# Optimization experiments

Hardware: AMD Instinct MI355X
Metric: run time of the kernel (lower is better)

Reference implementation:

```python
import jax, jax.numpy as jnp
import numpy as np

B, T, D, H, R = 4, 4096, 1024, 16, 256
DH = D // H  # 64


def setup_inputs() -> dict:
    key = jax.random.key(0)
    ks = jax.random.split(key, 5)
    s = 0.02
    return {
        "x": jax.random.normal(ks[0], (B, T, D), dtype=jnp.float32),
        "Wq": jax.random.normal(ks[1], (D, D), dtype=jnp.float32) * s,
        "bq": jnp.zeros((D,), dtype=jnp.float32),
        "Wd": jax.random.normal(ks[2], (D, R), dtype=jnp.float32) * s,
        "bd": jnp.zeros((R,), dtype=jnp.float32),
        "Wu": jax.random.normal(ks[3], (R, 2 * D), dtype=jnp.float32) * s,
        "bu": jnp.zeros((2 * D,), dtype=jnp.float32),
        "Wo": jax.random.normal(ks[4], (D, D), dtype=jnp.float32) * s,
        "bo": jnp.zeros((D,), dtype=jnp.float32),
    }


def reference(x, Wq, bq, Wd, bd, Wu, bu, Wo, bo):
    b, t = x.shape[0], x.shape[1]
    # q projection -> (B,T,H,DH)
    q = (x @ Wq + bq).reshape(b, t, H, DH)
    # low-rank KV: down then up -> (B,T,H,2*DH)
    kv = ((x @ Wd + bd) @ Wu + bu).reshape(b, t, H, 2 * DH)
    k, v = kv[..., :DH], kv[..., DH:]
    # elu+1 feature map
    q = jax.nn.elu(q) + 1.0
    k = jax.nn.elu(k) + 1.0
    # linear attention: context = k^T v per head -> (B,H,DH,DH)
    context = jnp.einsum("bthd,bthe->bhde", k, v)
    out = jnp.einsum("bthd,bhde->bthe", q, context)  # (B,T,H,DH)
    # normalizer: q . sum_t(k)
    k_sum = k.sum(axis=1)  # (B,H,DH)
    z = 1.0 / (jnp.einsum("bthd,bhd->bth", q, k_sum) + 1e-6)
    out = out * z[..., None]
    return out.reshape(b, t, D) @ Wo + bo
```

## Files before the change

kernel.cpp:

```cpp
#include <hip/hip_runtime.h>
#include <hip/hip_bf16.h>
#include <cstddef>
#include <cstdint>

#define B_  4
#define T_  4096
#define D_  1024
#define H_  16
#define DH_ 64
#define R_  256
#define BT_ (B_ * T_)
#define TWO_D_ (2 * D_)

typedef __attribute__((ext_vector_type(8))) short short8;
typedef __attribute__((ext_vector_type(4))) float f32x4;

__device__ __forceinline__ float elu1(float x) {
    return x > 0.0f ? x + 1.0f : __expf(x);
}

__device__ __forceinline__ float bf2f(short u) {
    union { uint32_t i; float f; } c;
    c.i = ((uint32_t)(uint16_t)u) << 16;
    return c.f;
}

typedef __attribute__((address_space(1))) void void_g;
typedef __attribute__((address_space(3))) void void_l;
__device__ __forceinline__ void gld_lds16(const void* g, void* l) {
    __builtin_amdgcn_global_load_lds(
        (const void_g*)(uintptr_t)g,
        (void_l*)(uint32_t)(uintptr_t)l,
        16, 0, 0);
}

__device__ __forceinline__ void store_out(float* p, float v) { *p = v; }
__device__ __forceinline__ void store_out(__hip_bfloat16* p, float v) { *p = __float2bfloat16(v); }

#define PBM 256
#define PBN 256

template<int EPI, bool BROW, typename OT>
__global__ __launch_bounds__(512, 2) void gemm_p8(
    const __hip_bfloat16* __restrict__ A,
    const __hip_bfloat16* __restrict__ Bt,
    const float* __restrict__ bias,
    OT* __restrict__ C,
    int M, int N, int K)
{
    __shared__ alignas(16) __hip_bfloat16 sm[65536];
    __hip_bfloat16* Asm = sm;
    __hip_bfloat16* Bsm = sm + 32768;

    const int nbx = N / PBN;
    const int nbm = M / PBM;
    const int sh = (nbm < 8) ? nbm : 8;
    const int id = blockIdx.x;
    const int wi = id % (sh * nbx);
    const int bm = ((id / (sh * nbx)) * sh + (wi % sh)) * PBM;
    const int bn = (wi / sh) * PBN;

    const int tid  = threadIdx.x;
    const int lane = tid & 63;
    const int w    = tid >> 6;
    const int wm   = w >> 2;
    const int wn   = w & 3;
    const int r15  = lane & 15;
    const int kg   = lane >> 4;

    const int nt = K / 64;

    const int rl = tid >> 3;
    const int g  = (tid & 7) ^ (rl & 7);
    const __hip_bfloat16* aS = A  + (size_t)(bm + rl) * K + g * 8;
    const __hip_bfloat16* bS = Bt + (size_t)(bn + rl) * K + g * 8;
    __hip_bfloat16* dA = Asm + tid * 8;
    __hip_bfloat16* dB = Bsm + tid * 8;

    auto stA = [&](int t, int h) {
        const int tc = (t < nt) ? t : (nt - 1);
        __hip_bfloat16* d = dA + ((t & 1) * 2 + h) * 8192;
        const __hip_bfloat16* s = aS + (size_t)(h * 128) * K + tc * 64;
        gld_lds16(s, d);
        gld_lds16(s + (size_t)64 * K, d + 4096);
    };
    auto stB = [&](int t, int h) {
        const int tc = (t < nt) ? t : (nt - 1);
        __hip_bfloat16* d = dB + ((t & 1) * 2 + h) * 8192;
        const __hip_bfloat16* s = bS + (size_t)(h * 128) * K + tc * 64;
        gld_lds16(s, d);
        gld_lds16(s + (size_t)64 * K, d + 4096);
    };

    const int x3    = (r15 & 7) << 3;
    const int kofs0 = (kg * 8) ^ x3;
    const int kofs1 = (32 + kg * 8) ^ x3;
    const __hip_bfloat16* Af0 = Asm + wm * 8192 + r15 * 64;
    const __hip_bfloat16* Bf0 = Bsm + (wn >> 1) * 8192 + (wn & 1) * 4096 + r15 * 64;
    const __hip_bfloat16* Af1 = Af0 + 16384;
    const __hip_bfloat16* Bf1 = Bf0 + 16384;

    f32x4 acc[8][4] = {};
    short8 af[8][2], bf[4][2];

#define RDA(i, ks, BASE) af[i][ks] = *(const short8*)((BASE) + (i) * 1024 + ((ks) ? kofs1 : kofs0))
#define RDB(j, ks, BASE) bf[j][ks] = *(const short8*)((BASE) + (j) * 1024 + ((ks) ? kofs1 : kofs0))
#define MM(ILO, IHI, JLO, JHI, KS)                                             \
    _Pragma("unroll")                                                          \
    for (int i = (ILO); i < (IHI); ++i)                                        \
        _Pragma("unroll")                                                      \
        for (int j = (JLO); j < (JHI); ++j)                                    \
            acc[i][j] = __builtin_amdgcn_mfma_f32_16x16x32_bf16(af[i][KS], bf[j][KS], acc[i][j], 0, 0, 0)
#define SB0() __builtin_amdgcn_sched_barrier(0)

    stA(0, 0); stA(0, 1); stB(0, 0); stB(0, 1); stA(1, 0); stA(1, 1);
    asm volatile("s_waitcnt vmcnt(4)" ::: "memory");
    __builtin_amdgcn_s_barrier();

    for (int t = 0; t < nt; t += 2) {
#pragma unroll
        for (int i = 0; i < 4; ++i) RDA(i, 0, Af0);
#pragma unroll
        for (int j = 0; j < 2; ++j) RDB(j, 0, Bf0);
        SB0();
#pragma unroll
        for (int i = 0; i < 4; ++i) RDA(i, 1, Af0);
#pragma unroll
        for (int j = 0; j < 2; ++j) RDB(j, 1, Bf0);
        stB(t + 1, 0);
        __builtin_amdgcn_s_barrier();
        asm volatile("s_waitcnt lgkmcnt(6)" ::: "memory");
        SB0();
        __builtin_amdgcn_s_setprio(1);
        MM(0, 4, 0, 2, 0);
        asm volatile("s_waitcnt lgkmcnt(0)" ::: "memory");
        SB0();
        MM(0, 4, 0, 2, 1);
        __builtin_amdgcn_s_setprio(0);
        __builtin_amdgcn_s_barrier();

#pragma unroll
        for (int i = 4; i < 8; ++i) RDA(i, 0, Af0);
        SB0();
#pragma unroll
        for (int i = 4; i < 8; ++i) RDA(i, 1, Af0);
        stB(t + 1, 1);
        __builtin_amdgcn_s_barrier();
        asm volatile("s_waitcnt lgkmcnt(4)" ::: "memory");
        SB0();
        __builtin_amdgcn_s_setprio(1);
        MM(4, 8, 0, 2, 0);
        asm volatile("s_waitcnt lgkmcnt(0)" ::: "memory");
        SB0();
        MM(4, 8, 0, 2, 1);
        __builtin_amdgcn_s_setprio(0);
        __builtin_amdgcn_s_barrier();

#pragma unroll
        for (int j = 2; j < 4; ++j) RDB(j, 0, Bf0);
        SB0();
#pragma unroll
        for (int j = 2; j < 4; ++j) RDB(j, 1, Bf0);
        stA(t + 2, 0);
        __builtin_amdgcn_s_barrier();
        asm volatile("s_waitcnt lgkmcnt(2)" ::: "memory");
        SB0();
        __builtin_amdgcn_s_setprio(1);
        MM(4, 8, 2, 4, 0);
        asm volatile("s_waitcnt lgkmcnt(0)" ::: "memory");
        SB0();
        MM(4, 8, 2, 4, 1);
        __builtin_amdgcn_s_setprio(0);
        __builtin_amdgcn_s_barrier();

        stA(t + 2, 1);
        asm volatile("s_waitcnt vmcnt(4)" ::: "memory");
        __builtin_amdgcn_s_barrier();
        SB0();
        __builtin_amdgcn_s_setprio(1);
        MM(0, 4, 2, 4, 0);
        MM(0, 4, 2, 4, 1);
        __builtin_amdgcn_s_setprio(0);
        __builtin_amdgcn_s_barrier();

#pragma unroll
        for (int i = 0; i < 4; ++i) RDA(i, 0, Af1);
#pragma unroll
        for (int j = 0; j < 2; ++j) RDB(j, 0, Bf1);
        SB0();
#pragma unroll
        for (int i = 0; i < 4; ++i) RDA(i, 1, Af1);
#pragma unroll
        for (int j = 0; j < 2; ++j) RDB(j, 1, Bf1);
        stB(t + 2, 0);
        __builtin_amdgcn_s_barrier();
        asm volatile("s_waitcnt lgkmcnt(6)" ::: "memory");
        SB0();
        __builtin_amdgcn_s_setprio(1);
        MM(0, 4, 0, 2, 0);
        asm volatile("s_waitcnt lgkmcnt(0)" ::: "memory");
        SB0();
        MM(0, 4, 0, 2, 1);
        __builtin_amdgcn_s_setprio(0);
        __builtin_amdgcn_s_barrier();

#pragma unroll
        for (int i = 4; i < 8; ++i) RDA(i, 0, Af1);
        SB0();
#pragma unroll
        for (int i = 4; i < 8; ++i) RDA(i, 1, Af1);
        stB(t + 2, 1);
        __builtin_amdgcn_s_barrier();
        asm volatile("s_waitcnt lgkmcnt(4)" ::: "memory");
        SB0();
        __builtin_amdgcn_s_setprio(1);
        MM(4, 8, 0, 2, 0);
        asm volatile("s_waitcnt lgkmcnt(0)" ::: "memory");
        SB0();
        MM(4, 8, 0, 2, 1);
        __builtin_amdgcn_s_setprio(0);
        __builtin_amdgcn_s_barrier();

#pragma unroll
        for (int j = 2; j < 4; ++j) RDB(j, 0, Bf1);
        SB0();
#pragma unroll
        for (int j = 2; j < 4; ++j) RDB(j, 1, Bf1);
        stA(t + 3, 0);
        __builtin_amdgcn_s_barrier();
        asm volatile("s_waitcnt lgkmcnt(2)" ::: "memory");
        SB0();
        __builtin_amdgcn_s_setprio(1);
        MM(4, 8, 2, 4, 0);
        asm volatile("s_waitcnt lgkmcnt(0)" ::: "memory");
        SB0();
        MM(4, 8, 2, 4, 1);
        __builtin_amdgcn_s_setprio(0);
        __builtin_amdgcn_s_barrier();

        stA(t + 3, 1);
        asm volatile("s_waitcnt vmcnt(4)" ::: "memory");
        __builtin_amdgcn_s_barrier();
        SB0();
        __builtin_amdgcn_s_setprio(1);
        MM(0, 4, 2, 4, 0);
        MM(0, 4, 2, 4, 1);
        __builtin_amdgcn_s_setprio(0);
        __builtin_amdgcn_s_barrier();
    }
    asm volatile("s_waitcnt vmcnt(0)" ::: "memory");

#undef RDA
#undef RDB
#undef MM
#undef SB0

    const int row0 = bm + wm * 128 + (lane >> 4) * 4;

    float brow[8][4];
    if (BROW) {
#pragma unroll
        for (int i = 0; i < 8; ++i)
#pragma unroll
            for (int r = 0; r < 4; ++r) brow[i][r] = bias[row0 + i * 16 + r];
    }
#pragma unroll
    for (int j = 0; j < 4; ++j) {
        const int col = bn + wn * 64 + j * 16 + r15;
        const float bv = BROW ? 0.0f : bias[col];
        const bool kp_col = ((col & 127) < 64);
#pragma unroll
        for (int i = 0; i < 8; ++i) {
#pragma unroll
            for (int r = 0; r < 4; ++r) {
                const int row = row0 + i * 16 + r;
                float v = acc[i][j][r] + (BROW ? brow[i][r] : bv);
                if (EPI == 1) v = elu1(v);
                else if (EPI == 2) {
                    const bool kp = BROW ? ((row & 127) < 64) : kp_col;
                    if (kp) v = elu1(v);
                }
                store_out(C + (size_t)row * N + col, v);
            }
        }
    }
}

#define BM 128
#define BN 128
#define BK 32
#define NBUF 5

template<int EPI, bool BROW, typename OT>
__global__ __launch_bounds__(256) void gemm_bf16(
    const __hip_bfloat16* __restrict__ A,
    const __hip_bfloat16* __restrict__ Bt,
    const float* __restrict__ bias,
    OT* __restrict__ C,
    OT* __restrict__ C2,
    int M, int N, int K)
{
    __shared__ alignas(16) __hip_bfloat16 As[NBUF * BM * BK];
    __shared__ alignas(16) __hip_bfloat16 Bs[NBUF * BN * BK];

    const int nbx = N / BN;
    const int id = blockIdx.x;
    const int strip = id / (8 * nbx);
    const int wi = id % (8 * nbx);
    const int bm = (strip * 8 + (wi & 7)) * BM;
    const int bn = (wi >> 3) * BN;

    const int tid  = threadIdx.x;
    const int lane = tid & 63;
    const int wm   = (tid >> 7) * 64;
    const int wn   = ((tid >> 6) & 1) * 64;
    const int r15  = lane & 15;
    const int kg   = lane >> 4;

    f32x4 acc[4][4] = {};

    const int c0 = tid, c1 = tid + 256;
    const __hip_bfloat16* a0 = A  + (size_t)(bm + (c0 >> 2)) * K + (c0 & 3) * 8;
    const __hip_bfloat16* a1 = A  + (size_t)(bm + (c1 >> 2)) * K + (c1 & 3) * 8;
    const __hip_bfloat16* b0 = Bt + (size_t)(bn + (c0 >> 2)) * K + (c0 & 3) * 8;
    const __hip_bfloat16* b1 = Bt + (size_t)(bn + (c1 >> 2)) * K + (c1 & 3) * 8;

    const int nk = K / BK;

    auto stage = [&](int t) {
        const int buf = t % NBUF;
        __hip_bfloat16* Ad = As + buf * (BM * BK);
        __hip_bfloat16* Bd = Bs + buf * (BN * BK);
        const int k0 = t * BK;
        gld_lds16(a0 + k0, Ad + c0 * 8);
        gld_lds16(a1 + k0, Ad + c1 * 8);
        gld_lds16(b0 + k0, Bd + c0 * 8);
        gld_lds16(b1 + k0, Bd + c1 * 8);
    };

    stage(0); stage(1); stage(2);

    for (int t = 0; t < nk; ++t) {
        if (t + 3 < nk) {
            stage(t + 3);
            asm volatile("s_waitcnt vmcnt(12)\ns_barrier" ::: "memory");
        } else if (t + 2 < nk) {
            asm volatile("s_waitcnt vmcnt(8)\ns_barrier" ::: "memory");
        } else if (t + 1 < nk) {
            asm volatile("s_waitcnt vmcnt(4)\ns_barrier" ::: "memory");
        } else {
            asm volatile("s_waitcnt vmcnt(0)\ns_barrier" ::: "memory");
        }

        const __hip_bfloat16* Asb = As + (t % NBUF) * (BM * BK);
        const __hip_bfloat16* Bsb = Bs + (t % NBUF) * (BN * BK);

        short8 af[4], bf[4];
#pragma unroll
        for (int i = 0; i < 4; ++i) {
            af[i] = *(const short8*)(Asb + (wm + i * 16 + r15) * BK + kg * 8);
            bf[i] = *(const short8*)(Bsb + (wn + i * 16 + r15) * BK + kg * 8);
        }
#pragma unroll
        for (int i = 0; i < 4; ++i)
#pragma unroll
            for (int j = 0; j < 4; ++j)
                acc[i][j] = __builtin_amdgcn_mfma_f32_16x16x32_bf16(af[i], bf[j], acc[i][j], 0, 0, 0);
    }

    const int row0 = bm + wm + (lane >> 4) * 4;

    if (EPI == 3) {
        const bool qreg = (bn < 1024);
#pragma unroll
        for (int j = 0; j < 4; ++j) {
            const int col = bn + wn + j * 16 + r15;
            const float bv = bias[col];
#pragma unroll
            for (int i = 0; i < 4; ++i)
#pragma unroll
                for (int r = 0; r < 4; ++r) {
                    const int row = row0 + i * 16 + r;
                    float v = acc[i][j][r] + bv;
                    if (qreg) {
                        store_out(C + (size_t)row * 1024 + col, elu1(v));
                    } else {
                        store_out(C2 + (size_t)row * 256 + (col - 1024), v);
                    }
                }
        }
        return;
    }

    float brow[4][4];
    if (BROW) {
#pragma unroll
        for (int i = 0; i < 4; ++i)
#pragma unroll
            for (int r = 0; r < 4; ++r) brow[i][r] = bias[row0 + i * 16 + r];
    }
#pragma unroll
    for (int j = 0; j < 4; ++j) {
        const int col = bn + wn + j * 16 + r15;
        const float bv = BROW ? 0.0f : bias[col];
        const bool kp_col = ((col & 127) < 64);
#pragma unroll
        for (int i = 0; i < 4; ++i) {
#pragma unroll
            for (int r = 0; r < 4; ++r) {
                const int row = row0 + i * 16 + r;
                float v = acc[i][j][r] + (BROW ? brow[i][r] : bv);
                if (EPI == 1) v = elu1(v);
                else if (EPI == 2) {
                    const bool kp = BROW ? ((row & 127) < 64) : kp_col;
                    if (kp) v = elu1(v);
                }
                store_out(C + (size_t)row * N + col, v);
            }
        }
    }
}

__device__ __forceinline__ void tcast_body(
    const float* __restrict__ W, __hip_bfloat16* __restrict__ Wt,
    int K, int N, int bx, int by, int tid, float (*t)[33])
{
    const int n0 = bx * 32, k0 = by * 32;
    const int c = tid & 31, r = tid >> 5;
#pragma unroll
    for (int rr = r; rr < 32; rr += 8)
        t[rr][c] = W[(size_t)(k0 + rr) * N + n0 + c];
    __syncthreads();
#pragma unroll
    for (int rr = r; rr < 32; rr += 8)
        Wt[(size_t)(n0 + rr) * K + k0 + c] = __float2bfloat16(t[c][rr]);
}

__global__ __launch_bounds__(256) void prep(
    const float* __restrict__ x,
    const float* __restrict__ Wq, const float* __restrict__ Wd,
    const float* __restrict__ Wu, const float* __restrict__ Wo,
    __hip_bfloat16* __restrict__ xb,
    __hip_bfloat16* __restrict__ WqdT, __hip_bfloat16* __restrict__ WuT,
    __hip_bfloat16* __restrict__ WoT,
    float* __restrict__ zbase)
{
    __shared__ float t[32][33];
    const int id = blockIdx.x;
    const int tid = threadIdx.x;

    if (id < 8192) {
        const int i = (id * 256 + tid) * 8;
        float4 v0 = *(const float4*)(x + i);
        float4 v1 = *(const float4*)(x + i + 4);
        __hip_bfloat16 tt[8];
        tt[0] = __float2bfloat16(v0.x); tt[1] = __float2bfloat16(v0.y);
        tt[2] = __float2bfloat16(v0.z); tt[3] = __float2bfloat16(v0.w);
        tt[4] = __float2bfloat16(v1.x); tt[5] = __float2bfloat16(v1.y);
        tt[6] = __float2bfloat16(v1.z); tt[7] = __float2bfloat16(v1.w);
        *(short8*)(xb + i) = *(const short8*)tt;
    } else if (id < 8192 + 1024) {
        const int u = id - 8192;
        tcast_body(Wq, WqdT, D_, D_, u & 31, u >> 5, tid, t);
    } else if (id < 8192 + 1280) {
        const int u = id - (8192 + 1024);
        tcast_body(Wd, WqdT + (size_t)D_ * D_, D_, R_, u & 7, u >> 3, tid, t);
    } else if (id < 8192 + 1792) {
        const int u = id - (8192 + 1280);
        tcast_body(Wu, WuT, R_, TWO_D_, u & 63, u >> 6, tid, t);
    } else if (id < 8192 + 2816) {
        const int u = id - (8192 + 1792);
        tcast_body(Wo, WoT, D_, D_, u & 31, u >> 5, tid, t);
    } else {
        const int u = id - (8192 + 2816);
        const int i = (u * 256 + tid) * 8;
        float4 z = {0.f, 0.f, 0.f, 0.f};
        *(float4*)(zbase + i) = z;
        *(float4*)(zbase + i + 4) = z;
    }
}

#define CHT 512

__global__ __launch_bounds__(256) void ctx_mfma(
    const __hip_bfloat16* __restrict__ kvT, float* __restrict__ ctx,
    float* __restrict__ ksum)
{
    __shared__ alignas(16) unsigned char smem[40960];
    float* red0 = (float*)smem;
    float* red1 = (float*)(smem + 20480);

    const int bh = blockIdx.x >> 3;
    const int chunk = blockIdx.x & 7;
    const int b = bh >> 4;
    const int h = bh & 15;
    const int tid = threadIdx.x;
    const int lane = tid & 63;
    const int w = tid >> 6;
    const int r15 = lane & 15;
    const int kg  = lane >> 4;

    f32x4 acc[4][4] = {};
    f32x4 acc4[4] = {};

    const short one = (short)0x3F80;
    const short8 bfv = (r15 == 0)
        ? (short8){one, one, one, one, one, one, one, one}
        : (short8){0, 0, 0, 0, 0, 0, 0, 0};

    const size_t tbase = (size_t)b * T_ + (size_t)chunk * CHT;
    const __hip_bfloat16* src = kvT + (size_t)(h * 128) * BT_ + tbase;

    for (int it = 0; it < CHT / 128; ++it) {
#pragma unroll
        for (int r = 0; r < 8; ++r) {
            const int c = r * 256 + tid;
            const int s = c >> 9, j = (c >> 2) & 127, u = c & 3;
            gld_lds16(src + (size_t)j * BT_ + it * 128 + s * 32 + u * 8,
                      smem + c * 16);
        }
        __syncthreads();

        const __hip_bfloat16* Ls = (const __hip_bfloat16*)smem;
        short8 af[4], bf[4];
#pragma unroll
        for (int i = 0; i < 4; ++i) {
            af[i] = *(const short8*)(Ls + (w * 128 + i * 16 + r15) * 32 + kg * 8);
            bf[i] = *(const short8*)(Ls + (w * 128 + 64 + i * 16 + r15) * 32 + kg * 8);
        }
#pragma unroll
        for (int i = 0; i < 4; ++i) {
#pragma unroll
            for (int j = 0; j < 4; ++j)
                acc[i][j] = __builtin_amdgcn_mfma_f32_16x16x32_bf16(af[i], bf[j], acc[i][j], 0, 0, 0);
            acc4[i] = __builtin_amdgcn_mfma_f32_16x16x32_bf16(af[i], bfv, acc4[i], 0, 0, 0);
        }
        __syncthreads();
    }

    const int q4 = lane >> 4;
    auto wr = [&](float* reg) {
#pragma unroll
        for (int i = 0; i < 4; ++i) {
#pragma unroll
            for (int r = 0; r < 4; ++r) {
                const int row = i * 16 + q4 * 4 + r;
#pragma unroll
                for (int j = 0; j < 4; ++j) reg[row * 80 + j * 16 + r15] = acc[i][j][r];
                reg[row * 80 + 64 + r15] = acc4[i][r];
            }
        }
    };
    auto rd = [&](const float* reg) {
#pragma unroll
        for (int i = 0; i < 4; ++i) {
#pragma unroll
            for (int r = 0; r < 4; ++r) {
                const int row = i * 16 + q4 * 4 + r;
#pragma unroll
                for (int j = 0; j < 4; ++j) acc[i][j][r] += reg[row * 80 + j * 16 + r15];
                acc4[i][r] += reg[row * 80 + 64 + r15];
            }
        }
    };

    if (w == 1) wr(red0);
    if (w == 3) wr(red1);
    __syncthreads();
    if (w == 0) rd(red0);
    if (w == 2) rd(red1);
    __syncthreads();
    if (w == 2) wr(red0);
    __syncthreads();
    if (w == 0) { rd(red0); wr(red0); }
    __syncthreads();

    float* cdst = ctx + (size_t)bh * 4096;
#pragma unroll
    for (int r = 0; r < 16; ++r) {
        const int idx = r * 256 + tid;
        const int d = idx >> 6, e = idx & 63;
        atomicAdd(cdst + idx, red0[d * 80 + e]);
    }
    if (tid < 64) atomicAdd(ksum + bh * 64 + tid, red0[tid * 80 + 64]);
}

__global__ __launch_bounds__(256) void pack_ctx(
    const float* __restrict__ ctx, __hip_bfloat16* __restrict__ ctxT)
{
    __shared__ float L[64 * 65];
    const int bh = blockIdx.x;
    const int tid = threadIdx.x;
#pragma unroll
    for (int r = 0; r < 16; ++r) {
        const int idx = r * 256 + tid;
        L[(idx >> 6) * 65 + (idx & 63)] = ctx[(size_t)bh * 4096 + idx];
    }
    __syncthreads();
#pragma unroll
    for (int r = 0; r < 16; ++r) {
        const int idx = r * 256 + tid;
        ctxT[(size_t)bh * 4096 + idx] =
            __float2bfloat16(L[(idx & 63) * 65 + (idx >> 6)]);
    }
}

__global__ __launch_bounds__(256) void out_mfma(
    const __hip_bfloat16* __restrict__ qb, const __hip_bfloat16* __restrict__ ctxT,
    const float* __restrict__ ksum, __hip_bfloat16* __restrict__ outb)
{
    __shared__ alignas(16) unsigned char As[256 * 128];
    __shared__ alignas(16) unsigned char Bs[64 * 128];
    __shared__ float ksumL[64];
    __shared__ float zbuf[256];

    const int bh = blockIdx.x >> 4;
    const int tile = blockIdx.x & 15;
    const int b = bh >> 4;
    const int h = bh & 15;
    const int tid = threadIdx.x;
    const int lane = tid & 63;
    const int w = tid >> 6;
    const int r15 = lane & 15;
    const int kg  = lane >> 4;

    const size_t trow0 = (size_t)b * T_ + (size_t)tile * 256;

#pragma unroll
    for (int r = 0; r < 8; ++r) {
        const int c = r * 256 + tid;
        const int row = c >> 3, slot = c & 7, u = slot ^ (row & 7);
        gld_lds16(qb + (trow0 + row) * D_ + h * 64 + u * 8, As + c * 16);
    }
#pragma unroll
    for (int r = 0; r < 2; ++r) {
        const int c = r * 256 + tid;
        const int row = c >> 3, slot = c & 7, u = slot ^ (row & 7);
        gld_lds16(ctxT + (size_t)bh * 4096 + row * 64 + u * 8, Bs + c * 16);
    }
    if (tid < 64) ksumL[tid] = ksum[bh * 64 + tid];
    __syncthreads();

    short8 af[4][2], bf[4][2];
#pragma unroll
    for (int i = 0; i < 4; ++i)
#pragma unroll
        for (int s = 0; s < 2; ++s) {
            const int m = w * 64 + i * 16 + r15;
            const int n = i * 16 + r15;
            const int uk = s * 4 + kg;
            af[i][s] = *(const short8*)(As + m * 128 + ((uk ^ (m & 7)) * 16));
            bf[i][s] = *(const short8*)(Bs + n * 128 + ((uk ^ (n & 7)) * 16));
        }

    f32x4 acc[4][4] = {};
#pragma unroll
    for (int s = 0; s < 2; ++s)
#pragma unroll
        for (int i = 0; i < 4; ++i)
#pragma unroll
            for (int j = 0; j < 4; ++j)
                acc[i][j] = __builtin_amdgcn_mfma_f32_16x16x32_bf16(af[i][s], bf[j][s], acc[i][j], 0, 0, 0);

    float dsum[4];
#pragma unroll
    for (int i = 0; i < 4; ++i) {
        float s0 = 0.0f;
#pragma unroll
        for (int s = 0; s < 2; ++s)
#pragma unroll
            for (int j8 = 0; j8 < 8; ++j8)
                s0 += bf2f(af[i][s][j8]) * ksumL[s * 32 + kg * 8 + j8];
        s0 += __shfl_xor(s0, 16);
        s0 += __shfl_xor(s0, 32);
        dsum[i] = s0;
    }
    if (lane < 16) {
#pragma unroll
        for (int i = 0; i < 4; ++i)
            zbuf[w * 64 + i * 16 + lane] = 1.0f / (dsum[i] + 1e-6f);
    }
    __syncthreads();

    const int q4 = lane >> 4;
#pragma unroll
    for (int i = 0; i < 4; ++i) {
#pragma unroll
        for (int r = 0; r < 4; ++r) {
            const int m = w * 64 + i * 16 + q4 * 4 + r;
            const float z = zbuf[m];
#pragma unroll
            for (int j = 0; j < 4; ++j) {
                outb[(trow0 + m) * D_ + h * 64 + j * 16 + r15] =
                    __float2bfloat16(acc[i][j][r] * z);
            }
        }
    }
}

extern "C" void kernel_launch(void* const* d_in, const int* in_sizes, int n_in,
                              void* d_out, int out_size, void* d_ws, size_t ws_size,
                              hipStream_t stream) {
    const float* x  = (const float*)d_in[0];
    const float* Wq = (const float*)d_in[1];
    const float* bq = (const float*)d_in[2];
    const float* Wd = (const float*)d_in[3];
    const float* bd = (const float*)d_in[4];
    const float* Wu = (const float*)d_in[5];
    const float* bu = (const float*)d_in[6];
    const float* Wo = (const float*)d_in[7];
    const float* bo = (const float*)d_in[8];
    float* out = (float*)d_out;

    __hip_bfloat16* xb    = (__hip_bfloat16*)d_ws;
    __hip_bfloat16* WqdT  = xb    + (size_t)BT_ * D_;
    __hip_bfloat16* WuT   = WqdT  + (size_t)1280 * D_;
    __hip_bfloat16* WoT   = WuT   + (size_t)TWO_D_ * R_;
    __hip_bfloat16* xdb   = WoT   + (size_t)D_ * D_;
    __hip_bfloat16* kvT   = xdb   + (size_t)BT_ * R_;
    __hip_bfloat16* qb    = kvT   + (size_t)TWO_D_ * BT_;
    float* bias_qd = (float*)(qb + (size_t)BT_ * D_);
    float* ctx  = bias_qd + 1280;
    float* ksum = ctx + (size_t)B_ * H_ * DH_ * DH_;
    __hip_bfloat16* ctxT = (__hip_bfloat16*)(ksum + B_ * H_ * DH_);
    __hip_bfloat16* outb = xb;

    prep<<<8192 + 2816 + 130, 256, 0, stream>>>(
        x, Wq, Wd, Wu, Wo, xb, WqdT, WuT, WoT, ctx);

    gemm_bf16<0, false, __hip_bfloat16><<<(BT_ / BM) * (R_ / BN), 256, 0, stream>>>(
        xb, WqdT + (size_t)D_ * D_, bd, xdb, nullptr, BT_, R_, D_);
    gemm_p8<1, false, __hip_bfloat16><<<(BT_ / PBM) * (D_ / PBN), 512, 0, stream>>>(
        xb, WqdT, bq, qb, BT_, D_, D_);
    gemm_p8<2, true, __hip_bfloat16><<<(TWO_D_ / PBM) * (BT_ / PBN), 512, 0, stream>>>(
        WuT, xdb, bu, kvT, TWO_D_, BT_, R_);
    ctx_mfma<<<64 * (T_ / CHT), 256, 0, stream>>>(kvT, ctx, ksum);
    pack_ctx<<<64, 256, 0, stream>>>(ctx, ctxT);
    out_mfma<<<64 * 16, 256, 0, stream>>>(qb, ctxT, ksum, outb);
    gemm_p8<0, false, float><<<(BT_ / PBM) * (D_ / PBN), 512, 0, stream>>>(
        outb, WoT, bo, out, BT_, D_, D_);
}
```

Measured before the change: 311.8 us.

## Fuse KV up-projection GEMM with per-head context reduction

Replaces the KV up-projection GEMM, its kvT global write, and the separate ctx_mfma kernel with one kernel. After the GEMM main loop, each 256x256 tile applies the bias and elu+1, stages the tile in LDS as bf16, and computes the partial k^T v and k-sum with MFMA. The partials are then atomically added into ctx and ksum. This removes the write and reread of the large kvT intermediate and one kernel launch. In exchange there are many more float atomics (one set per 256-token tile) and an extra LDS epilogue phase per block.

```diff
diff --git a/kernel.cpp b/kernel.cpp
--- a/kernel.cpp
+++ b/kernel.cpp
@@ -39,6 +39,142 @@
 
 #define PBM 256
 #define PBN 256
+
+#define RDA(i, ks, BASE) af[i][ks] = *(const short8*)((BASE) + (i) * 1024 + ((ks) ? kofs1 : kofs0))
+#define RDB(j, ks, BASE) bf[j][ks] = *(const short8*)((BASE) + (j) * 1024 + ((ks) ? kofs1 : kofs0))
+#define MM(ILO, IHI, JLO, JHI, KS)                                             \
+    _Pragma("unroll")                                                          \
+    for (int i = (ILO); i < (IHI); ++i)                                        \
+        _Pragma("unroll")                                                      \
+        for (int j = (JLO); j < (JHI); ++j)                                    \
+            acc[i][j] = __builtin_amdgcn_mfma_f32_16x16x32_bf16(af[i][KS], bf[j][KS], acc[i][j], 0, 0, 0)
+#define SB0() __builtin_amdgcn_sched_barrier(0)
+
+#define P8_KLOOP(AF0, BF0, AF1, BF1)                                           \
+    for (int t = 0; t < nt; t += 2) {                                          \
+        _Pragma("unroll")                                                      \
+        for (int i = 0; i < 4; ++i) RDA(i, 0, AF0);                            \
+        _Pragma("unroll")                                                      \
+        for (int j = 0; j < 2; ++j) RDB(j, 0, BF0);                            \
+        SB0();                                                                 \
+        _Pragma("unroll")                                                      \
+        for (int i = 0; i < 4; ++i) RDA(i, 1, AF0);                            \
+        _Pragma("unroll")                                                      \
+        for (int j = 0; j < 2; ++j) RDB(j, 1, BF0);                            \
+        stB(t + 1, 0);                                                         \
+        __builtin_amdgcn_s_barrier();                                          \
+        asm volatile("s_waitcnt lgkmcnt(6)" ::: "memory");                     \
+        SB0();                                                                 \
+        __builtin_amdgcn_s_setprio(1);                                         \
+        MM(0, 4, 0, 2, 0);                                                     \
+        asm volatile("s_waitcnt lgkmcnt(0)" ::: "memory");                     \
+        SB0();                                                                 \
+        MM(0, 4, 0, 2, 1);                                                     \
+        __builtin_amdgcn_s_setprio(0);                                         \
+        __builtin_amdgcn_s_barrier();                                          \
+        _Pragma("unroll")                                                      \
+        for (int i = 4; i < 8; ++i) RDA(i, 0, AF0);                            \
+        SB0();                                                                 \
+        _Pragma("unroll")                                                      \
+        for (int i = 4; i < 8; ++i) RDA(i, 1, AF0);                            \
+        stB(t + 1, 1);                                                         \
+        __builtin_amdgcn_s_barrier();                                          \
+        asm volatile("s_waitcnt lgkmcnt(4)" ::: "memory");                     \
+        SB0();                                                                 \
+        __builtin_amdgcn_s_setprio(1);                                         \
+        MM(4, 8, 0, 2, 0);                                                     \
+        asm volatile("s_waitcnt lgkmcnt(0)" ::: "memory");                     \
+        SB0();                                                                 \
+        MM(4, 8, 0, 2, 1);                                                     \
+        __builtin_amdgcn_s_setprio(0);                                         \
+        __builtin_amdgcn_s_barrier();                                          \
+        _Pragma("unroll")                                                      \
+        for (int j = 2; j < 4; ++j) RDB(j, 0, BF0);                            \
+        SB0();                                                                 \
+        _Pragma("unroll")                                                      \
+        for (int j = 2; j < 4; ++j) RDB(j, 1, BF0);                            \
+        stA(t + 2, 0);                                                         \
+        __builtin_amdgcn_s_barrier();                                          \
+        asm volatile("s_waitcnt lgkmcnt(2)" ::: "memory");                     \
+        SB0();                                                                 \
+        __builtin_amdgcn_s_setprio(1);                                         \
+        MM(4, 8, 2, 4, 0);                                                     \
+        asm volatile("s_waitcnt lgkmcnt(0)" ::: "memory");                     \
+        SB0();                                                                 \
+        MM(4, 8, 2, 4, 1);                                                     \
+        __builtin_amdgcn_s_setprio(0);                                         \
+        __builtin_amdgcn_s_barrier();                                          \
+        stA(t + 2, 1);                                                         \
+        asm volatile("s_waitcnt vmcnt(4)" ::: "memory");                       \
+        __builtin_amdgcn_s_barrier();                                          \
+        SB0();                                                                 \
+        __builtin_amdgcn_s_setprio(1);                                         \
+        MM(0, 4, 2, 4, 0);                                                     \
+        MM(0, 4, 2, 4, 1);                                                     \
+        __builtin_amdgcn_s_setprio(0);                                         \
+        __builtin_amdgcn_s_barrier();                                          \
+        _Pragma("unroll")                                                      \
+        for (int i = 0; i < 4; ++i) RDA(i, 0, AF1);                            \
+        _Pragma("unroll")                                                      \
+        for (int j = 0; j < 2; ++j) RDB(j, 0, BF1);                            \
+        SB0();                                                                 \
+        _Pragma("unroll")                                                      \
+        for (int i = 0; i < 4; ++i) RDA(i, 1, AF1);                            \
+        _Pragma("unroll")                                                      \
+        for (int j = 0; j < 2; ++j) RDB(j, 1, BF1);                            \
+        stB(t + 2, 0);                                                         \
+        __builtin_amdgcn_s_barrier();                                          \
+        asm volatile("s_waitcnt lgkmcnt(6)" ::: "memory");                     \
+        SB0();                                                                 \
+        __builtin_amdgcn_s_setprio(1);                                         \
+        MM(0, 4, 0, 2, 0);                                                     \
+        asm volatile("s_waitcnt lgkmcnt(0)" ::: "memory");                     \
+        SB0();                                                                 \
+        MM(0, 4, 0, 2, 1);                                                     \
+        __builtin_amdgcn_s_setprio(0);                                         \
+        __builtin_amdgcn_s_barrier();                                          \
+        _Pragma("unroll")                                                      \
+        for (int i = 4; i < 8; ++i) RDA(i, 0, AF1);                            \
+        SB0();                                                                 \
+        _Pragma("unroll")                                                      \
+        for (int i = 4; i < 8; ++i) RDA(i, 1, AF1);                            \
+        stB(t + 2, 1);                                                         \
+        __builtin_amdgcn_s_barrier();                                          \
+        asm volatile("s_waitcnt lgkmcnt(4)" ::: "memory");                     \
+        SB0();                                                                 \
+        __builtin_amdgcn_s_setprio(1);                                         \
+        MM(4, 8, 0, 2, 0);                                                     \
+        asm volatile("s_waitcnt lgkmcnt(0)" ::: "memory");                     \
+        SB0();                                                                 \
+        MM(4, 8, 0, 2, 1);                                                     \
+        __builtin_amdgcn_s_setprio(0);                                         \
+        __builtin_amdgcn_s_barrier();                                          \
+        _Pragma("unroll")                                                      \
+        for (int j = 2; j < 4; ++j) RDB(j, 0, BF1);                            \
+        SB0();                                                                 \
+        _Pragma("unroll")                                                      \
+        for (int j = 2; j < 4; ++j) RDB(j, 1, BF1);                            \
+        stA(t + 3, 0);                                                         \
+        __builtin_amdgcn_s_barrier();                                          \
+        asm volatile("s_waitcnt lgkmcnt(2)" ::: "memory");                     \
+        SB0();                                                                 \
+        __builtin_amdgcn_s_setprio(1);                                         \
+        MM(4, 8, 2, 4, 0);                                                     \
+        asm volatile("s_waitcnt lgkmcnt(0)" ::: "memory");                     \
+        SB0();                                                                 \
+        MM(4, 8, 2, 4, 1);                                                     \
+        __builtin_amdgcn_s_setprio(0);                                         \
+        __builtin_amdgcn_s_barrier();                                          \
+        stA(t + 3, 1);                                                         \
+        asm volatile("s_waitcnt vmcnt(4)" ::: "memory");                       \
+        __builtin_amdgcn_s_barrier();                                          \
+        SB0();                                                                 \
+        __builtin_amdgcn_s_setprio(1);                                         \
+        MM(0, 4, 2, 4, 0);                                                     \
+        MM(0, 4, 2, 4, 1);                                                     \
+        __builtin_amdgcn_s_setprio(0);                                         \
+        __builtin_amdgcn_s_barrier();                                          \
+    }
 
 template<int EPI, bool BROW, typename OT>
 __global__ __launch_bounds__(512, 2) void gemm_p8(
@@ -103,157 +239,13 @@
     f32x4 acc[8][4] = {};
     short8 af[8][2], bf[4][2];
 
-#define RDA(i, ks, BASE) af[i][ks] = *(const short8*)((BASE) + (i) * 1024 + ((ks) ? kofs1 : kofs0))
-#define RDB(j, ks, BASE) bf[j][ks] = *(const short8*)((BASE) + (j) * 1024 + ((ks) ? kofs1 : kofs0))
-#define MM(ILO, IHI, JLO, JHI, KS)                                             \
-    _Pragma("unroll")                                                          \
-    for (int i = (ILO); i < (IHI); ++i)                                        \
-        _Pragma("unroll")                                                      \
-        for (int j = (JLO); j < (JHI); ++j)                                    \
-            acc[i][j] = __builtin_amdgcn_mfma_f32_16x16x32_bf16(af[i][KS], bf[j][KS], acc[i][j], 0, 0, 0)
-#define SB0() __builtin_amdgcn_sched_barrier(0)
-
     stA(0, 0); stA(0, 1); stB(0, 0); stB(0, 1); stA(1, 0); stA(1, 1);
     asm volatile("s_waitcnt vmcnt(4)" ::: "memory");
     __builtin_amdgcn_s_barrier();
 
-    for (int t = 0; t < nt; t += 2) {
-#pragma unroll
-        for (int i = 0; i < 4; ++i) RDA(i, 0, Af0);
-#pragma unroll
-        for (int j = 0; j < 2; ++j) RDB(j, 0, Bf0);
-        SB0();
-#pragma unroll
-        for (int i = 0; i < 4; ++i) RDA(i, 1, Af0);
-#pragma unroll
-        for (int j = 0; j < 2; ++j) RDB(j, 1, Bf0);
-        stB(t + 1, 0);
-        __builtin_amdgcn_s_barrier();
-        asm volatile("s_waitcnt lgkmcnt(6)" ::: "memory");
-        SB0();
-        __builtin_amdgcn_s_setprio(1);
-        MM(0, 4, 0, 2, 0);
-        asm volatile("s_waitcnt lgkmcnt(0)" ::: "memory");
-        SB0();
-        MM(0, 4, 0, 2, 1);
-        __builtin_amdgcn_s_setprio(0);
-        __builtin_amdgcn_s_barrier();
-
-#pragma unroll
-        for (int i = 4; i < 8; ++i) RDA(i, 0, Af0);
-        SB0();
-#pragma unroll
-        for (int i = 4; i < 8; ++i) RDA(i, 1, Af0);
-        stB(t + 1, 1);
-        __builtin_amdgcn_s_barrier();
-        asm volatile("s_waitcnt lgkmcnt(4)" ::: "memory");
-        SB0();
-        __builtin_amdgcn_s_setprio(1);
-        MM(4, 8, 0, 2, 0);
-        asm volatile("s_waitcnt lgkmcnt(0)" ::: "memory");
-        SB0();
-        MM(4, 8, 0, 2, 1);
-        __builtin_amdgcn_s_setprio(0);
-        __builtin_amdgcn_s_barrier();
-
-#pragma unroll
-        for (int j = 2; j < 4; ++j) RDB(j, 0, Bf0);
-        SB0();
-#pragma unroll
-        for (int j = 2; j < 4; ++j) RDB(j, 1, Bf0);
-        stA(t + 2, 0);
-        __builtin_amdgcn_s_barrier();
-        asm volatile("s_waitcnt lgkmcnt(2)" ::: "memory");
-        SB0();
-        __builtin_amdgcn_s_setprio(1);
-        MM(4, 8, 2, 4, 0);
-        asm volatile("s_waitcnt lgkmcnt(0)" ::: "memory");
-        SB0();
-        MM(4, 8, 2, 4, 1);
-        __builtin_amdgcn_s_setprio(0);
-        __builtin_amdgcn_s_barrier();
-
-        stA(t + 2, 1);
-        asm volatile("s_waitcnt vmcnt(4)" ::: "memory");
-        __builtin_amdgcn_s_barrier();
-        SB0();
-        __builtin_amdgcn_s_setprio(1);
-        MM(0, 4, 2, 4, 0);
-        MM(0, 4, 2, 4, 1);
-        __builtin_amdgcn_s_setprio(0);
-        __builtin_amdgcn_s_barrier();
-
-#pragma unroll
-        for (int i = 0; i < 4; ++i) RDA(i, 0, Af1);
-#pragma unroll
-        for (int j = 0; j < 2; ++j) RDB(j, 0, Bf1);
-        SB0();
-#pragma unroll
-        for (int i = 0; i < 4; ++i) RDA(i, 1, Af1);
-#pragma unroll
-        for (int j = 0; j < 2; ++j) RDB(j, 1, Bf1);
-        stB(t + 2, 0);
-        __builtin_amdgcn_s_barrier();
-        asm volatile("s_waitcnt lgkmcnt(6)" ::: "memory");
-        SB0();
-        __builtin_amdgcn_s_setprio(1);
-        MM(0, 4, 0, 2, 0);
-        asm volatile("s_waitcnt lgkmcnt(0)" ::: "memory");
-        SB0();
-        MM(0, 4, 0, 2, 1);
-        __builtin_amdgcn_s_setprio(0);
-        __builtin_amdgcn_s_barrier();
-
-#pragma unroll
-        for (int i = 4; i < 8; ++i) RDA(i, 0, Af1);
-        SB0();
-#pragma unroll
-        for (int i = 4; i < 8; ++i) RDA(i, 1, Af1);
-        stB(t + 2, 1);
-        __builtin_amdgcn_s_barrier();
-        asm volatile("s_waitcnt lgkmcnt(4)" ::: "memory");
-        SB0();
-        __builtin_amdgcn_s_setprio(1);
-        MM(4, 8, 0, 2, 0);
-        asm volatile("s_waitcnt lgkmcnt(0)" ::: "memory");
-        SB0();
-        MM(4, 8, 0, 2, 1);
-        __builtin_amdgcn_s_setprio(0);
-        __builtin_amdgcn_s_barrier();
-
-#pragma unroll
-        for (int j = 2; j < 4; ++j) RDB(j, 0, Bf1);
-        SB0();
-#pragma unroll
-        for (int j = 2; j < 4; ++j) RDB(j, 1, Bf1);
-        stA(t + 3, 0);
-        __builtin_amdgcn_s_barrier();
-        asm volatile("s_waitcnt lgkmcnt(2)" ::: "memory");
-        SB0();
-        __builtin_amdgcn_s_setprio(1);
-        MM(4, 8, 2, 4, 0);
-        asm volatile("s_waitcnt lgkmcnt(0)" ::: "memory");
-        SB0();
-        MM(4, 8, 2, 4, 1);
-        __builtin_amdgcn_s_setprio(0);
-        __builtin_amdgcn_s_barrier();
-
-        stA(t + 3, 1);
-        asm volatile("s_waitcnt vmcnt(4)" ::: "memory");
-        __builtin_amdgcn_s_barrier();
-        SB0();
-        __builtin_amdgcn_s_setprio(1);
-        MM(0, 4, 2, 4, 0);
-        MM(0, 4, 2, 4, 1);
-        __builtin_amdgcn_s_setprio(0);
-        __builtin_amdgcn_s_barrier();
-    }
+    P8_KLOOP(Af0, Bf0, Af1, Bf1)
+
     asm volatile("s_waitcnt vmcnt(0)" ::: "memory");
-
-#undef RDA
-#undef RDB
-#undef MM
-#undef SB0
 
     const int row0 = bm + wm * 128 + (lane >> 4) * 4;
 
@@ -285,6 +277,158 @@
         }
     }
 }
+
+__global__ __launch_bounds__(512, 2) void gemm3_ctx(
+    const __hip_bfloat16* __restrict__ A,
+    const __hip_bfloat16* __restrict__ Bt,
+    const float* __restrict__ bias,
+    float* __restrict__ ctx, float* __restrict__ ksum,
+    int M, int N, int K)
+{
+    __shared__ alignas(16) __hip_bfloat16 sm[65536];
+    __hip_bfloat16* Asm = sm;
+    __hip_bfloat16* Bsm = sm + 32768;
+
+    const int nbx = N / PBN;
+    const int nbm = M / PBM;
+    const int sh = (nbm < 8) ? nbm : 8;
+    const int id = blockIdx.x;
+    const int wi = id % (sh * nbx);
+    const int bm = ((id / (sh * nbx)) * sh + (wi % sh)) * PBM;
+    const int bn = (wi / sh) * PBN;
+
+    const int tid  = threadIdx.x;
+    const int lane = tid & 63;
+    const int w    = tid >> 6;
+    const int wm   = w >> 2;
+    const int wn   = w & 3;
+    const int r15  = lane & 15;
+    const int kg   = lane >> 4;
+
+    const int nt = K / 64;
+
+    const int rl = tid >> 3;
+    const int g  = (tid & 7) ^ (rl & 7);
+    const __hip_bfloat16* aS = A  + (size_t)(bm + rl) * K + g * 8;
+    const __hip_bfloat16* bS = Bt + (size_t)(bn + rl) * K + g * 8;
+    __hip_bfloat16* dA = Asm + tid * 8;
+    __hip_bfloat16* dB = Bsm + tid * 8;
+
+    auto stA = [&](int t, int h) {
+        const int tc = (t < nt) ? t : (nt - 1);
+        __hip_bfloat16* d = dA + ((t & 1) * 2 + h) * 8192;
+        const __hip_bfloat16* s = aS + (size_t)(h * 128) * K + tc * 64;
+        gld_lds16(s, d);
+        gld_lds16(s + (size_t)64 * K, d + 4096);
+    };
+    auto stB = [&](int t, int h) {
+        const int tc = (t < nt) ? t : (nt - 1);
+        __hip_bfloat16* d = dB + ((t & 1) * 2 + h) * 8192;
+        const __hip_bfloat16* s = bS + (size_t)(h * 128) * K + tc * 64;
+        gld_lds16(s, d);
+        gld_lds16(s + (size_t)64 * K, d + 4096);
+    };
+
+    const int x3    = (r15 & 7) << 3;
+    const int kofs0 = (kg * 8) ^ x3;
+    const int kofs1 = (32 + kg * 8) ^ x3;
+    const __hip_bfloat16* Af0 = Asm + wm * 8192 + r15 * 64;
+    const __hip_bfloat16* Bf0 = Bsm + (wn >> 1) * 8192 + (wn & 1) * 4096 + r15 * 64;
+    const __hip_bfloat16* Af1 = Af0 + 16384;
+    const __hip_bfloat16* Bf1 = Bf0 + 16384;
+
+    f32x4 acc[8][4] = {};
+    short8 af[8][2], bf[4][2];
+
+    stA(0, 0); stA(0, 1); stB(0, 0); stB(0, 1); stA(1, 0); stA(1, 1);
+    asm volatile("s_waitcnt vmcnt(4)" ::: "memory");
+    __builtin_amdgcn_s_barrier();
+
+    P8_KLOOP(Af0, Bf0, Af1, Bf1)
+
+    asm volatile("s_waitcnt vmcnt(0)" ::: "memory");
+    __syncthreads();
+
+    __hip_bfloat16* Lt = sm;
+    {
+        const int jb0 = wm * 128 + (lane >> 4) * 4;
+        float brow[8][4];
+#pragma unroll
+        for (int i = 0; i < 8; ++i)
+#pragma unroll
+            for (int r = 0; r < 4; ++r) brow[i][r] = bias[bm + jb0 + i * 16 + r];
+#pragma unroll
+        for (int i = 0; i < 8; ++i)
+#pragma unroll
+            for (int r = 0; r < 4; ++r) {
+                const int j = jb0 + i * 16 + r;
+                const bool kp = (j & 127) < 64;
+#pragma unroll
+                for (int jj = 0; jj < 4; ++jj) {
+                    const int t = wn * 64 + jj * 16 + r15;
+                    float v = acc[i][jj][r] + brow[i][r];
+                    if (kp) v = elu1(v);
+                    Lt[j * 256 + (((t >> 3) ^ (j & 7)) * 8) + (t & 7)] =
+                        __float2bfloat16(v);
+                }
+            }
+    }
+    __syncthreads();
+
+    const int hh = w >> 2, di = (w >> 1) & 1, ei = w & 1;
+    const short one = (short)0x3F80;
+    const short8 bfv = (r15 == 0)
+        ? (short8){one, one, one, one, one, one, one, one}
+        : (short8){0, 0, 0, 0, 0, 0, 0, 0};
+    f32x4 cacc[2][2] = {};
+    f32x4 kacc[2] = {};
+#pragma unroll
+    for (int ks = 0; ks < 8; ++ks) {
+        short8 kf[2], vf[2];
+#pragma unroll
+        for (int i2 = 0; i2 < 2; ++i2) {
+            const int jA = hh * 128 + di * 32 + i2 * 16 + r15;
+            kf[i2] = *(const short8*)(Lt + jA * 256 + (((ks * 4 + kg) ^ (jA & 7)) * 8));
+            const int jV = hh * 128 + 64 + ei * 32 + i2 * 16 + r15;
+            vf[i2] = *(const short8*)(Lt + jV * 256 + (((ks * 4 + kg) ^ (jV & 7)) * 8));
+        }
+#pragma unroll
+        for (int i2 = 0; i2 < 2; ++i2) {
+#pragma unroll
+            for (int j2 = 0; j2 < 2; ++j2)
+                cacc[i2][j2] = __builtin_amdgcn_mfma_f32_16x16x32_bf16(kf[i2], vf[j2], cacc[i2][j2], 0, 0, 0);
+            if (ei == 0)
+                kacc[i2] = __builtin_amdgcn_mfma_f32_16x16x32_bf16(kf[i2], bfv, kacc[i2], 0, 0, 0);
+        }
+    }
+
+    const int bh = ((bn >> 12) << 4) + (bm >> 7) + hh;
+    float* cd = ctx + (size_t)bh * 4096;
+    const int q4 = lane >> 4;
+#pragma unroll
+    for (int i2 = 0; i2 < 2; ++i2)
+#pragma unroll
+        for (int j2 = 0; j2 < 2; ++j2)
+#pragma unroll
+            for (int r = 0; r < 4; ++r) {
+                const int d = di * 32 + i2 * 16 + q4 * 4 + r;
+                const int e = ei * 32 + j2 * 16 + r15;
+                atomicAdd(cd + d * 64 + e, cacc[i2][j2][r]);
+            }
+    if (ei == 0 && r15 == 0) {
+#pragma unroll
+        for (int i2 = 0; i2 < 2; ++i2)
+#pragma unroll
+            for (int r = 0; r < 4; ++r)
+                atomicAdd(ksum + bh * 64 + di * 32 + i2 * 16 + q4 * 4 + r,
+                          kacc[i2][r]);
+    }
+}
+
+#undef RDA
+#undef RDB
+#undef MM
+#undef SB0
 
 #define BM 128
 #define BN 128
@@ -480,111 +624,6 @@
     }
 }
 
-#define CHT 512
-
-__global__ __launch_bounds__(256) void ctx_mfma(
-    const __hip_bfloat16* __restrict__ kvT, float* __restrict__ ctx,
-    float* __restrict__ ksum)
-{
-    __shared__ alignas(16) unsigned char smem[40960];
-    float* red0 = (float*)smem;
-    float* red1 = (float*)(smem + 20480);
-
-    const int bh = blockIdx.x >> 3;
-    const int chunk = blockIdx.x & 7;
-    const int b = bh >> 4;
-    const int h = bh & 15;
-    const int tid = threadIdx.x;
-    const int lane = tid & 63;
-    const int w = tid >> 6;
-    const int r15 = lane & 15;
-    const int kg  = lane >> 4;
-
-    f32x4 acc[4][4] = {};
-    f32x4 acc4[4] = {};
-
-    const short one = (short)0x3F80;
-    const short8 bfv = (r15 == 0)
-        ? (short8){one, one, one, one, one, one, one, one}
-        : (short8){0, 0, 0, 0, 0, 0, 0, 0};
-
-    const size_t tbase = (size_t)b * T_ + (size_t)chunk * CHT;
-    const __hip_bfloat16* src = kvT + (size_t)(h * 128) * BT_ + tbase;
-
-    for (int it = 0; it < CHT / 128; ++it) {
-#pragma unroll
-        for (int r = 0; r < 8; ++r) {
-            const int c = r * 256 + tid;
-            const int s = c >> 9, j = (c >> 2) & 127, u = c & 3;
-            gld_lds16(src + (size_t)j * BT_ + it * 128 + s * 32 + u * 8,
-                      smem + c * 16);
-        }
-        __syncthreads();
-
-        const __hip_bfloat16* Ls = (const __hip_bfloat16*)smem;
-        short8 af[4], bf[4];
-#pragma unroll
-        for (int i = 0; i < 4; ++i) {
-            af[i] = *(const short8*)(Ls + (w * 128 + i * 16 + r15) * 32 + kg * 8);
-            bf[i] = *(const short8*)(Ls + (w * 128 + 64 + i * 16 + r15) * 32 + kg * 8);
-        }
-#pragma unroll
-        for (int i = 0; i < 4; ++i) {
-#pragma unroll
-            for (int j = 0; j < 4; ++j)
-                acc[i][j] = __builtin_amdgcn_mfma_f32_16x16x32_bf16(af[i], bf[j], acc[i][j], 0, 0, 0);
-            acc4[i] = __builtin_amdgcn_mfma_f32_16x16x32_bf16(af[i], bfv, acc4[i], 0, 0, 0);
-        }
-        __syncthreads();
-    }
-
-    const int q4 = lane >> 4;
-    auto wr = [&](float* reg) {
-#pragma unroll
-        for (int i = 0; i < 4; ++i) {
-#pragma unroll
-            for (int r = 0; r < 4; ++r) {
-                const int row = i * 16 + q4 * 4 + r;
-#pragma unroll
-                for (int j = 0; j < 4; ++j) reg[row * 80 + j * 16 + r15] = acc[i][j][r];
-                reg[row * 80 + 64 + r15] = acc4[i][r];
-            }
-        }
-    };
-    auto rd = [&](const float* reg) {
-#pragma unroll
-        for (int i = 0; i < 4; ++i) {
-#pragma unroll
-            for (int r = 0; r < 4; ++r) {
-                const int row = i * 16 + q4 * 4 + r;
-#pragma unroll
-                for (int j = 0; j < 4; ++j) acc[i][j][r] += reg[row * 80 + j * 16 + r15];
-                acc4[i][r] += reg[row * 80 + 64 + r15];
-            }
-        }
-    };
-
-    if (w == 1) wr(red0);
-    if (w == 3) wr(red1);
-    __syncthreads();
-    if (w == 0) rd(red0);
-    if (w == 2) rd(red1);
-    __syncthreads();
-    if (w == 2) wr(red0);
-    __syncthreads();
-    if (w == 0) { rd(red0); wr(red0); }
-    __syncthreads();
-
-    float* cdst = ctx + (size_t)bh * 4096;
-#pragma unroll
-    for (int r = 0; r < 16; ++r) {
-        const int idx = r * 256 + tid;
-        const int d = idx >> 6, e = idx & 63;
-        atomicAdd(cdst + idx, red0[d * 80 + e]);
-    }
-    if (tid < 64) atomicAdd(ksum + bh * 64 + tid, red0[tid * 80 + 64]);
-}
-
 __global__ __launch_bounds__(256) void pack_ctx(
     const float* __restrict__ ctx, __hip_bfloat16* __restrict__ ctxT)
 {
@@ -732,9 +771,8 @@
         xb, WqdT + (size_t)D_ * D_, bd, xdb, nullptr, BT_, R_, D_);
     gemm_p8<1, false, __hip_bfloat16><<<(BT_ / PBM) * (D_ / PBN), 512, 0, stream>>>(
         xb, WqdT, bq, qb, BT_, D_, D_);
-    gemm_p8<2, true, __hip_bfloat16><<<(TWO_D_ / PBM) * (BT_ / PBN), 512, 0, stream>>>(
-        WuT, xdb, bu, kvT, TWO_D_, BT_, R_);
-    ctx_mfma<<<64 * (T_ / CHT), 256, 0, stream>>>(kvT, ctx, ksum);
+    gemm3_ctx<<<(TWO_D_ / PBM) * (BT_ / PBN), 512, 0, stream>>>(
+        WuT, xdb, bu, ctx, ksum, TWO_D_, BT_, R_);
     pack_ctx<<<64, 256, 0, stream>>>(ctx, ctxT);
     out_mfma<<<64 * 16, 256, 0, stream>>>(qb, ctxT, ksum, outb);
     gemm_p8<0, false, float><<<(BT_ / PBM) * (D_ / PBN), 512, 0, stream>>>(
```

Result: faster. 300.8 us (-3.5%).
